# Kernel tuning notes

Hardware: AMD Instinct MI355X
Metric: run time of the kernel (lower is better)

The kernel has to match this reference:

```python
import jax, jax.numpy as jnp
import numpy as np

N, E, T, D = 50000, 800000, 400000, 64


def _linear_params(key, fan_in, fan_out):
    kw, kb = jax.random.split(key)
    s = 1.0 / np.sqrt(fan_in)
    W = jax.random.uniform(kw, (fan_in, fan_out), minval=-s, maxval=s, dtype=jnp.float32)
    b = jax.random.uniform(kb, (fan_out,), minval=-s, maxval=s, dtype=jnp.float32)
    return W, b


def setup_inputs() -> dict:
    key = jax.random.key(0)
    ks = jax.random.split(key, 11)
    Ws1, bs1 = _linear_params(ks[0], 2 * D, D)
    Ws2, bs2 = _linear_params(ks[1], D, 3 * D)
    Wc1, bc1 = _linear_params(ks[2], 2 * D, D)
    Wc2, bc2 = _linear_params(ks[3], D, D)
    WV, bV = _linear_params(ks[4], D, D)
    return {
        "node_scalar": jax.random.normal(ks[5], (N, D), dtype=jnp.float32),
        "node_chiral": jax.random.normal(ks[6], (N, D), dtype=jnp.float32),
        "node_vector": jax.random.normal(ks[7], (N, 3, D), dtype=jnp.float32),
        "pos": jax.random.normal(ks[8], (N, 3), dtype=jnp.float32),
        "edge_index": jax.random.randint(ks[9], (E, 2), 0, N, dtype=jnp.int64),
        "triplet_index": jax.random.randint(ks[10], (T, 4), 0, N, dtype=jnp.int64),
        "Ws1": Ws1, "bs1": bs1, "Ws2": Ws2, "bs2": bs2,
        "Wc1": Wc1, "bc1": bc1, "Wc2": Wc2, "bc2": bc2,
        "WV": WV, "bV": bV,
    }


def reference(node_scalar, node_chiral, node_vector, pos, edge_index, triplet_index,
              Ws1, bs1, Ws2, bs2, Wc1, bc1, Wc2, bc2, WV, bV):
    n = node_scalar.shape[0]
    d = node_scalar.shape[1]
    e0, e1 = edge_index[:, 0], edge_index[:, 1]

    # Scalar / vector section: gather -> Linear-SiLU-Linear gate -> scatter-add
    g = jax.nn.silu(jnp.concatenate([node_scalar[e0], node_scalar[e1]], axis=1) @ Ws1 + bs1) @ Ws2 + bs2
    gate_vector, gate_edge, messages_ss = jnp.split(g, 3, axis=1)  # each [E, d]
    messages_vv = gate_vector[:, None, :] * node_vector[e1]               # [E, 3, d]
    rel = pos[e1] - pos[e0]                                               # [E, 3]
    messages_ev = gate_edge[:, None, :] * rel[:, :, None]                 # [E, 3, d]
    msg_ss = jax.ops.segment_sum(messages_ss, e0, num_segments=n)
    msg_vv = jax.ops.segment_sum(messages_vv, e0, num_segments=n)
    msg_ev = jax.ops.segment_sum(messages_ev, e0, num_segments=n)

    Vv = node_vector @ WV + bV          # [N, 3, d]
    Vv_norm = jnp.linalg.norm(Vv, axis=1)  # [N, d] (norm over spatial axis)
    message_vs = node_scalar * Vv_norm

    # Chiral section: triplet gathers, shared gate MLP, scalar triple product
    base, t1, t2, t3 = (triplet_index[:, i] for i in range(4))
    hc_base = node_chiral[base]

    def cgate(other):
        h = jnp.concatenate([hc_base, node_chiral[other]], axis=1)
        return jax.nn.silu(h @ Wc1 + bc1) @ Wc2 + bc2

    chiral_gate = cgate(t1) + cgate(t2) + cgate(t3)  # [T, d]
    pb = pos[base]
    r1, r2, r3 = pb - pos[t1], pb - pos[t2], pb - pos[t3]
    stp = jnp.einsum('ei,ei->e', r1, jnp.cross(r2, r3))  # scalar triple product [T]
    chiral_messages = chiral_gate / (stp + 0.01)[:, None]
    msg_chiral = jax.ops.segment_sum(chiral_messages, base, num_segments=n)

    return (node_scalar + msg_ss + message_vs,
            node_chiral + msg_chiral,
            node_vector + msg_vv + msg_ev)
```

## Files before the change

### kernel.cpp

```cpp
#include <hip/hip_runtime.h>
#include <math.h>

#define DD 64
typedef unsigned short ushort_t;
typedef __attribute__((ext_vector_type(8))) short bf16x8;
typedef __attribute__((ext_vector_type(4))) float f32x4;

__device__ __forceinline__ float silu_f(float x) {
    return x / (1.0f + __expf(-x));
}

__device__ __forceinline__ unsigned f32_to_bf16_rne(float x) {
    unsigned u = __float_as_uint(x);
    unsigned r = ((u >> 16) & 1u) + 0x7fffu;
    return (u + r) >> 16;
}

__device__ __forceinline__ float bf16_to_f32(ushort_t v) {
    return __uint_as_float(((unsigned)v) << 16);
}

__device__ __forceinline__ float2 bf2_lo_hi(unsigned u) {
    return make_float2(__uint_as_float(u << 16), __uint_as_float(u & 0xffff0000u));
}

__device__ __forceinline__ void gload_lds4(const void* gsrc, void* lds_base) {
    __builtin_amdgcn_global_load_lds(
        (const __attribute__((address_space(1))) void*)gsrc,
        (__attribute__((address_space(3))) void*)lds_base,
        4, 0, 0);
}

#define RFL(x) __builtin_amdgcn_readfirstlane(x)

__global__ __launch_bounds__(256) void hist_kernel(const int* __restrict__ eidx,
                                                   int* __restrict__ counts, int E) {
    int i = blockIdx.x * 256 + threadIdx.x;
    if (i < E) atomicAdd(&counts[((const int2*)eidx)[i].x], 1);
}

__global__ __launch_bounds__(1024) void scan_kernel(const int* __restrict__ counts,
                                                    int* __restrict__ cursor, int N) {
    __shared__ int part[1024];
    int tid = threadIdx.x;
    int CH = (N + 1023) / 1024;
    int lo = tid * CH, hi = lo + CH; if (hi > N) hi = N; if (lo > N) lo = N;
    int s = 0;
    for (int i = lo; i < hi; ++i) s += counts[i];
    part[tid] = s;
    __syncthreads();
    for (int d = 1; d < 1024; d <<= 1) {
        int v = (tid >= d) ? part[tid - d] : 0;
        __syncthreads();
        part[tid] += v;
        __syncthreads();
    }
    int run = (tid == 0) ? 0 : part[tid - 1];
    for (int i = lo; i < hi; ++i) {
        cursor[i] = run;
        run += counts[i];
    }
}

__global__ __launch_bounds__(256) void scatter2_kernel(const int* __restrict__ eidx,
                                                       const float* __restrict__ pos,
                                                       int* __restrict__ cursor,
                                                       int2* __restrict__ eperm,
                                                       float* __restrict__ relg, int E) {
    int i = blockIdx.x * 256 + threadIdx.x;
    if (i < E) {
        int2 p = ((const int2*)eidx)[i];
        int dst = atomicAdd(&cursor[p.x], 1);
        eperm[dst] = p;
        relg[3 * (size_t)dst + 0] = pos[(size_t)p.y * 3 + 0] - pos[(size_t)p.x * 3 + 0];
        relg[3 * (size_t)dst + 1] = pos[(size_t)p.y * 3 + 1] - pos[(size_t)p.x * 3 + 1];
        relg[3 * (size_t)dst + 2] = pos[(size_t)p.y * 3 + 2] - pos[(size_t)p.x * 3 + 2];
    }
}

__global__ __launch_bounds__(256) void node_transform_kernel(
    const float* __restrict__ ns, const float* __restrict__ nc,
    const float* __restrict__ Ws1, const float* __restrict__ Wc1,
    ushort_t* __restrict__ Abf, ushort_t* __restrict__ Bbf,
    float* __restrict__ C, float* __restrict__ Dm,
    float* __restrict__ out1, int N)
{
    __shared__ float w1[128 * 64];
    __shared__ float wc1s[128 * 64];
    __shared__ float xs[4][2][64];
    __shared__ float ys[4][2][64];
    int tid = threadIdx.x;
    for (int i = tid; i < 128 * 64 / 4; i += 256) {
        ((float4*)w1)[i]   = ((const float4*)Ws1)[i];
        ((float4*)wc1s)[i] = ((const float4*)Wc1)[i];
    }
    __syncthreads();
    int wave = tid >> 6, lane = tid & 63;
    for (int nb = blockIdx.x * 8; nb < N; nb += gridDim.x * 8) {
        int n0 = nb + wave * 2;
        #pragma unroll
        for (int s = 0; s < 2; ++s) {
            int n = n0 + s;
            float xv = 0.f, yv = 0.f;
            if (n < N) { xv = ns[(size_t)n * DD + lane]; yv = nc[(size_t)n * DD + lane]; }
            xs[wave][s][lane] = xv;
            ys[wave][s][lane] = yv;
        }
        float aA[2] = {0.f, 0.f}, aB[2] = {0.f, 0.f}, aC[2] = {0.f, 0.f}, aD[2] = {0.f, 0.f};
        for (int k = 0; k < 64; ++k) {
            float wa  = w1[k * 64 + lane];
            float wb  = w1[(64 + k) * 64 + lane];
            float wca = wc1s[k * 64 + lane];
            float wcb = wc1s[(64 + k) * 64 + lane];
            #pragma unroll
            for (int s = 0; s < 2; ++s) {
                float xk = xs[wave][s][k];
                float yk = ys[wave][s][k];
                aA[s] += xk * wa;  aB[s] += xk * wb;
                aC[s] += yk * wca; aD[s] += yk * wcb;
            }
        }
        #pragma unroll
        for (int s = 0; s < 2; ++s) {
            int n = n0 + s;
            if (n < N) {
                Abf[(size_t)n * DD + lane] = (ushort_t)f32_to_bf16_rne(aA[s]);
                Bbf[(size_t)n * DD + lane] = (ushort_t)f32_to_bf16_rne(aB[s]);
                C[(size_t)n * DD + lane]  = aC[s];
                Dm[(size_t)n * DD + lane] = aD[s];
                out1[(size_t)n * DD + lane] = ys[wave][s][lane];
            }
        }
    }
}

__global__ __launch_bounds__(256) void node_vector_kernel(
    const float* __restrict__ ns, const float* __restrict__ nv,
    const float* __restrict__ WV, const float* __restrict__ bV,
    float* __restrict__ out0, float* __restrict__ out2,
    unsigned* __restrict__ nv01p, ushort_t* __restrict__ nv2bf, int N)
{
    __shared__ float wv[64 * 64];
    __shared__ float vs[4][2][3][64];
    int tid = threadIdx.x;
    for (int i = tid; i < 64 * 64 / 4; i += 256)
        ((float4*)wv)[i] = ((const float4*)WV)[i];
    __syncthreads();
    int wave = tid >> 6, lane = tid & 63;
    float bVj = bV[lane];
    for (int nb = blockIdx.x * 8; nb < N; nb += gridDim.x * 8) {
        int n0 = nb + wave * 2;
        #pragma unroll
        for (int s = 0; s < 2; ++s) {
            int n = n0 + s;
            float v0 = 0.f, v1 = 0.f, v2 = 0.f;
            if (n < N) {
                v0 = nv[((size_t)n * 3 + 0) * DD + lane];
                v1 = nv[((size_t)n * 3 + 1) * DD + lane];
                v2 = nv[((size_t)n * 3 + 2) * DD + lane];
            }
            vs[wave][s][0][lane] = v0; vs[wave][s][1][lane] = v1; vs[wave][s][2][lane] = v2;
        }
        float a0[2], a1[2], a2[2];
        #pragma unroll
        for (int s = 0; s < 2; ++s) { a0[s] = bVj; a1[s] = bVj; a2[s] = bVj; }
        for (int k = 0; k < 64; ++k) {
            float w = wv[k * 64 + lane];
            #pragma unroll
            for (int s = 0; s < 2; ++s) {
                a0[s] += vs[wave][s][0][k] * w;
                a1[s] += vs[wave][s][1][k] * w;
                a2[s] += vs[wave][s][2][k] * w;
            }
        }
        #pragma unroll
        for (int s = 0; s < 2; ++s) {
            int n = n0 + s;
            if (n < N) {
                float norm = sqrtf(a0[s] * a0[s] + a1[s] * a1[s] + a2[s] * a2[s]);
                float x = ns[(size_t)n * DD + lane];
                out0[(size_t)n * DD + lane] = x * (1.f + norm);
                float v0 = vs[wave][s][0][lane], v1 = vs[wave][s][1][lane], v2 = vs[wave][s][2][lane];
                out2[((size_t)n * 3 + 0) * DD + lane] = v0;
                out2[((size_t)n * 3 + 1) * DD + lane] = v1;
                out2[((size_t)n * 3 + 2) * DD + lane] = v2;
                nv01p[(size_t)n * DD + lane] = f32_to_bf16_rne(v0) | (f32_to_bf16_rne(v1) << 16);
                nv2bf[(size_t)n * DD + lane] = (ushort_t)f32_to_bf16_rne(v2);
            }
        }
    }
}

#define GEPW 16
__global__ __launch_bounds__(256) void edge_kernel(
    const ushort_t* __restrict__ Abf, const ushort_t* __restrict__ Bbf,
    const unsigned* __restrict__ nv01p, const ushort_t* __restrict__ nv2bf,
    const float* __restrict__ relg, const int2* __restrict__ eperm,
    const float* __restrict__ bs1, const float* __restrict__ Ws2, const float* __restrict__ bs2,
    float* __restrict__ out0, float* __restrict__ out2, int E)
{
    __shared__ unsigned w2frag[12 * 2 * 64 * 4];
    __shared__ ushort_t stAB[4][GEPW][128];
    __shared__ ushort_t stNV2[4][GEPW / 2][132];
    __shared__ float    relL[4][64];
    int tid = threadIdx.x;
    for (int i = tid; i < 12 * 2 * 64; i += 256) {
        int t  = i >> 7;
        int kk = (i >> 6) & 1;
        int l  = i & 63;
        int k0 = kk * 32 + (l >> 4) * 8;
        int col = t * 16 + (l & 15);
        #pragma unroll
        for (int jp = 0; jp < 4; ++jp) {
            float a = Ws2[(size_t)(k0 + 2 * jp) * 192 + col];
            float b = Ws2[(size_t)(k0 + 2 * jp + 1) * 192 + col];
            w2frag[i * 4 + jp] = f32_to_bf16_rne(a) | (f32_to_bf16_rne(b) << 16);
        }
    }
    __syncthreads();
    int wave = RFL(tid >> 6);
    int lane = tid & 63;
    float b1 = bs1[lane];
    float b2v_t[4], b2e_t[4], b2s_t[4];
    #pragma unroll
    for (int t = 0; t < 4; ++t) {
        b2v_t[t] = bs2[t * 16 + (lane & 15)];
        b2e_t[t] = bs2[64 + t * 16 + (lane & 15)];
        b2s_t[t] = bs2[128 + t * 16 + (lane & 15)];
    }

    int bid = blockIdx.x;
    int cpx = (int)(gridDim.x >> 3);
    int swz = (bid & 7) * cpx + (bid >> 3);

    long nG = ((long)E + GEPW - 1) / GEPW;
    for (long g = (long)swz * 4 + wave; g < nG; g += (long)gridDim.x * 4) {
        long e0b = g * GEPW;
        int i0a[GEPW], i1a[GEPW];
        #pragma unroll
        for (int e = 0; e < GEPW; ++e) {
            long eid = e0b + e; if (eid >= E) eid = E - 1;
            int2 p = eperm[eid];
            i0a[e] = RFL(p.x); i1a[e] = RFL(p.y);
        }
        int vi_all = 0, vi1_all = 0;
        #pragma unroll
        for (int e = 0; e < GEPW; ++e) {
            vi_all  = (lane == e) ? i0a[e] : vi_all;
            vi1_all = (lane == e) ? i1a[e] : vi1_all;
        }
        #pragma unroll
        for (int e = 0; e < GEPW; ++e) {
            const char* srcAB = (lane < 32)
                ? ((const char*)Abf + (size_t)i0a[e] * 128 + lane * 4)
                : ((const char*)Bbf + (size_t)i1a[e] * 128 + (lane - 32) * 4);
            gload_lds4(srcAB, &stAB[wave][e][0]);
        }
        __builtin_amdgcn_sched_barrier(0);
        #pragma unroll
        for (int p2 = 0; p2 < GEPW / 2; ++p2) {
            const char* src2 = (lane < 32)
                ? ((const char*)nv2bf + (size_t)i1a[2 * p2] * 128 + lane * 4)
                : ((const char*)nv2bf + (size_t)i1a[2 * p2 + 1] * 128 + (lane - 32) * 4);
            gload_lds4(src2, &stNV2[wave][p2][0]);
        }
        gload_lds4((const char*)relg + e0b * 12 + lane * 4, &relL[wave][0]);
        int eL0 = (lane >> 4) * 4;
        unsigned nv01r[4][4];
        #pragma unroll
        for (int rg = 0; rg < 4; ++rg) {
            int i1s = __builtin_amdgcn_ds_bpermute((eL0 + rg) * 4, vi1_all);
            const char* basep = (const char*)nv01p + (size_t)(unsigned)i1s * 256 + (lane & 15) * 4;
            nv01r[rg][0] = *(const unsigned*)(basep);
            nv01r[rg][1] = *(const unsigned*)(basep + 64);
            nv01r[rg][2] = *(const unsigned*)(basep + 128);
            nv01r[rg][3] = *(const unsigned*)(basep + 192);
        }
        __builtin_amdgcn_sched_barrier(0);
        asm volatile("s_waitcnt vmcnt(25)" ::: "memory");
        __builtin_amdgcn_sched_barrier(0);
        #pragma unroll
        for (int e = 0; e < GEPW; ++e) {
            float a = bf16_to_f32(stAB[wave][e][lane]);
            float b = bf16_to_f32(stAB[wave][e][64 + lane]);
            float h = silu_f(a + b + b1);
            *(float*)((char*)&stAB[wave][e][0] + ((lane * 4) ^ ((e & 7) << 5))) = h;
        }
        __builtin_amdgcn_sched_barrier(0);
        f32x4 acc[12];
        f32x4 zz = {0.f, 0.f, 0.f, 0.f};
        #pragma unroll
        for (int t = 0; t < 12; ++t) acc[t] = zz;
        int row = lane & 15;
        #pragma unroll
        for (int kk = 0; kk < 2; ++kk) {
            int coff = (kk * 128 + ((lane >> 4) * 32)) ^ ((row & 7) << 5);
            const char* hp = (const char*)&stAB[wave][row][0] + coff;
            float4 lo = *(const float4*)hp;
            float4 hi = *(const float4*)(hp + 16);
            unsigned a0, a1, a2, a3;
            asm("v_cvt_pk_bf16_f32 %0, %1, %2" : "=v"(a0) : "v"(lo.x), "v"(lo.y));
            asm("v_cvt_pk_bf16_f32 %0, %1, %2" : "=v"(a1) : "v"(lo.z), "v"(lo.w));
            asm("v_cvt_pk_bf16_f32 %0, %1, %2" : "=v"(a2) : "v"(hi.x), "v"(hi.y));
            asm("v_cvt_pk_bf16_f32 %0, %1, %2" : "=v"(a3) : "v"(hi.z), "v"(hi.w));
            union { unsigned u[4]; bf16x8 v; } af;
            af.u[0] = a0; af.u[1] = a1; af.u[2] = a2; af.u[3] = a3;
            #pragma unroll
            for (int t = 0; t < 12; ++t) {
                bf16x8 bf = *(const bf16x8*)&w2frag[((t * 2 + kk) * 64 + lane) * 4];
                acc[t] = __builtin_amdgcn_mfma_f32_16x16x32_bf16(af.v, bf, acc[t], 0, 0, 0);
            }
        }
        asm volatile("s_waitcnt vmcnt(0)" ::: "memory");
        __builtin_amdgcn_sched_barrier(0);
        float aS[4]  = {0.f, 0.f, 0.f, 0.f};
        float aV0[4] = {0.f, 0.f, 0.f, 0.f};
        float aV1[4] = {0.f, 0.f, 0.f, 0.f};
        float aV2[4] = {0.f, 0.f, 0.f, 0.f};
        int icur = __builtin_amdgcn_ds_bpermute(eL0 * 4, vi_all);
        #pragma unroll
        for (int rg = 0; rg < 4; ++rg) {
            int e = eL0 + rg;
            int i0 = __builtin_amdgcn_ds_bpermute(e * 4, vi_all);
            bool ok = (e0b + e) < E;
            if (i0 != icur) {
                #pragma unroll
                for (int t = 0; t < 4; ++t) {
                    int dim = t * 16 + (lane & 15);
                    unsafeAtomicAdd(&out0[(size_t)(unsigned)icur * 64u + dim], aS[t]);
                    unsafeAtomicAdd(&out2[((size_t)(unsigned)icur * 3u + 0) * 64u + dim], aV0[t]);
                    unsafeAtomicAdd(&out2[((size_t)(unsigned)icur * 3u + 1) * 64u + dim], aV1[t]);
                    unsafeAtomicAdd(&out2[((size_t)(unsigned)icur * 3u + 2) * 64u + dim], aV2[t]);
                    aS[t] = 0.f; aV0[t] = 0.f; aV1[t] = 0.f; aV2[t] = 0.f;
                }
                icur = i0;
            }
            if (ok) {
                float r0v = relL[wave][e * 3 + 0];
                float r1v = relL[wave][e * 3 + 1];
                float r2v = relL[wave][e * 3 + 2];
                #pragma unroll
                for (int t = 0; t < 4; ++t) {
                    int dim = t * 16 + (lane & 15);
                    float gv = acc[t][rg]     + b2v_t[t];
                    float ge = acc[4 + t][rg] + b2e_t[t];
                    float ss = acc[8 + t][rg] + b2s_t[t];
                    float2 vv = bf2_lo_hi(nv01r[rg][t]);
                    float v2 = bf16_to_f32(stNV2[wave][e >> 1][(e & 1) * 64 + dim]);
                    aS[t]  += ss;
                    aV0[t] += gv * vv.x + ge * r0v;
                    aV1[t] += gv * vv.y + ge * r1v;
                    aV2[t] += gv * v2   + ge * r2v;
                }
            }
        }
        #pragma unroll
        for (int t = 0; t < 4; ++t) {
            int dim = t * 16 + (lane & 15);
            unsafeAtomicAdd(&out0[(size_t)(unsigned)icur * 64u + dim], aS[t]);
            unsafeAtomicAdd(&out2[((size_t)(unsigned)icur * 3u + 0) * 64u + dim], aV0[t]);
            unsafeAtomicAdd(&out2[((size_t)(unsigned)icur * 3u + 1) * 64u + dim], aV1[t]);
            unsafeAtomicAdd(&out2[((size_t)(unsigned)icur * 3u + 2) * 64u + dim], aV2[t]);
        }
    }
}

#define TPW 8
__global__ __launch_bounds__(256) void triplet_kernel(
    const float* __restrict__ C, const float* __restrict__ Dm,
    const float* __restrict__ pos, const int* __restrict__ tidx,
    const float* __restrict__ bc1, const float* __restrict__ Wc2, const float* __restrict__ bc2,
    float* __restrict__ out1, int T)
{
    __shared__ float wT[64 * 64];
    __shared__ float stC[4][TPW][64];
    __shared__ float stD[4][TPW][3][64];
    int tid = threadIdx.x;
    for (int i = tid; i < 64 * 64 / 4; i += 256)
        ((float4*)wT)[i] = ((const float4*)Wc2)[i];
    __syncthreads();
    int wave = RFL(tid >> 6);
    int lane = tid & 63;
    float b1 = bc1[lane];
    float b2 = bc2[lane] * 3.0f;
    for (long bb = (long)blockIdx.x * (4 * TPW); bb < T; bb += (long)gridDim.x * (4 * TPW)) {
        long t0 = bb + wave * TPW;
        int ib[TPW], it1[TPW], it2[TPW], it3[TPW];
        #pragma unroll
        for (int e = 0; e < TPW; ++e) {
            long t = t0 + e;
            int b = 0, t1 = 0, t2 = 0, t3 = 0;
            if (t < T) { int4 q = ((const int4*)tidx)[t]; b = q.x; t1 = q.y; t2 = q.z; t3 = q.w; }
            ib[e]  = RFL(b);
            it1[e] = RFL(t1);
            it2[e] = RFL(t2);
            it3[e] = RFL(t3);
        }
        #pragma unroll
        for (int e = 0; e < TPW; ++e) {
            gload_lds4(C  + (size_t)ib[e]  * DD + lane, &stC[wave][e][0]);
            gload_lds4(Dm + (size_t)it1[e] * DD + lane, &stD[wave][e][0][0]);
            gload_lds4(Dm + (size_t)it2[e] * DD + lane, &stD[wave][e][1][0]);
            gload_lds4(Dm + (size_t)it3[e] * DD + lane, &stD[wave][e][2][0]);
        }
        asm volatile("s_waitcnt vmcnt(0)" ::: "memory");
        float inv[TPW];
        #pragma unroll
        for (int e = 0; e < TPW; ++e) {
            float hb = stC[wave][e][lane] + b1;
            float h = silu_f(hb + stD[wave][e][0][lane])
                    + silu_f(hb + stD[wave][e][1][lane])
                    + silu_f(hb + stD[wave][e][2][lane]);
            stC[wave][e][lane] = h;
            int b = ib[e], t1 = it1[e], t2 = it2[e], t3 = it3[e];
            double pbx = pos[(size_t)b * 3], pby = pos[(size_t)b * 3 + 1], pbz = pos[(size_t)b * 3 + 2];
            double r1x = pbx - pos[(size_t)t1 * 3], r1y = pby - pos[(size_t)t1 * 3 + 1], r1z = pbz - pos[(size_t)t1 * 3 + 2];
            double r2x = pbx - pos[(size_t)t2 * 3], r2y = pby - pos[(size_t)t2 * 3 + 1], r2z = pbz - pos[(size_t)t2 * 3 + 2];
            double r3x = pbx - pos[(size_t)t3 * 3], r3y = pby - pos[(size_t)t3 * 3 + 1], r3z = pbz - pos[(size_t)t3 * 3 + 2];
            double cx = r2y * r3z - r2z * r3y;
            double cy = r2z * r3x - r2x * r3z;
            double cz = r2x * r3y - r2y * r3x;
            double stp = r1x * cx + r1y * cy + r1z * cz;
            inv[e] = (float)(1.0 / (stp + 0.01));
        }
        float acc[TPW];
        #pragma unroll
        for (int e = 0; e < TPW; ++e) acc[e] = 0.f;
        for (int k4 = 0; k4 < 64; k4 += 4) {
            float4 hk[TPW];
            #pragma unroll
            for (int e = 0; e < TPW; ++e) hk[e] = *(const float4*)&stC[wave][e][k4];
            #pragma unroll
            for (int kk = 0; kk < 4; ++kk) {
                float wk = wT[(k4 + kk) * 64 + lane];
                #pragma unroll
                for (int e = 0; e < TPW; ++e) acc[e] += (&hk[e].x)[kk] * wk;
            }
        }
        #pragma unroll
        for (int e = 0; e < TPW; ++e) {
            long t = t0 + e;
            if (t >= T) break;
            unsafeAtomicAdd(&out1[(size_t)ib[e] * DD + lane], (acc[e] + b2) * inv[e]);
        }
    }
}

extern "C" void kernel_launch(void* const* d_in, const int* in_sizes, int n_in,
                              void* d_out, int out_size, void* d_ws, size_t ws_size,
                              hipStream_t stream)
{
    const float* ns  = (const float*)d_in[0];
    const float* nc  = (const float*)d_in[1];
    const float* nv  = (const float*)d_in[2];
    const float* pos = (const float*)d_in[3];
    const int* eidx  = (const int*)d_in[4];
    const int* tidx  = (const int*)d_in[5];
    const float* Ws1 = (const float*)d_in[6];
    const float* bs1 = (const float*)d_in[7];
    const float* Ws2 = (const float*)d_in[8];
    const float* bs2 = (const float*)d_in[9];
    const float* Wc1 = (const float*)d_in[10];
    const float* bc1 = (const float*)d_in[11];
    const float* Wc2 = (const float*)d_in[12];
    const float* bc2 = (const float*)d_in[13];
    const float* WV  = (const float*)d_in[14];
    const float* bV  = (const float*)d_in[15];

    int N = in_sizes[0] / 64;
    int E = in_sizes[4] / 2;
    int T = in_sizes[5] / 4;

    float* out0 = (float*)d_out;
    float* out1 = out0 + (size_t)N * 64;
    float* out2 = out1 + (size_t)N * 64;

    float* C    = (float*)d_ws;
    float* Dm   = C + (size_t)N * 64;
    float* relg = Dm + (size_t)N * 64;
    int2* eperm = (int2*)(relg + (size_t)E * 3 + 64);
    int* counts = (int*)(eperm + (size_t)E);
    int* cursor = counts + N;
    unsigned* nv01p = (unsigned*)(cursor + N);
    ushort_t* Abf   = (ushort_t*)(nv01p + (size_t)N * 64);
    ushort_t* Bbf   = Abf + (size_t)N * 64;
    ushort_t* nv2bf = Bbf + (size_t)N * 64;

    hipMemsetAsync(counts, 0, (size_t)N * sizeof(int), stream);
    hist_kernel<<<(E + 255) / 256, 256, 0, stream>>>(eidx, counts, E);
    scan_kernel<<<1, 1024, 0, stream>>>(counts, cursor, N);
    scatter2_kernel<<<(E + 255) / 256, 256, 0, stream>>>(eidx, pos, cursor, eperm, relg, E);
    node_transform_kernel<<<2048, 256, 0, stream>>>(ns, nc, Ws1, Wc1, Abf, Bbf, C, Dm, out1, N);
    node_vector_kernel<<<2048, 256, 0, stream>>>(ns, nv, WV, bV, out0, out2, nv01p, nv2bf, N);
    edge_kernel<<<4096, 256, 0, stream>>>(Abf, Bbf, nv01p, nv2bf, relg, eperm, bs1, Ws2, bs2, out0, out2, E);
    triplet_kernel<<<2048, 256, 0, stream>>>(C, Dm, pos, tidx, bc1, Wc2, bc2, out1, T);
}
```

Before: 953.6 us.

## Merge independent kernels into block-partitioned fused launches

Scatter, node-transform and node-vector kernels become one launch whose blocks pick a role by block index. The edge and triplet kernels are likewise merged into one launch, so independent work runs concurrently and fewer launches are needed. The cost is a large shared-memory footprint sized for the biggest role, which may lower occupancy for the lighter roles. The node loops also gain an extra __syncthreads per iteration.

Result: slower. 994.6 us (+4.3%).

```diff
diff --git a/kernel.cpp b/kernel.cpp
--- a/kernel.cpp
+++ b/kernel.cpp
@@ -5,6 +5,11 @@
 typedef unsigned short ushort_t;
 typedef __attribute__((ext_vector_type(8))) short bf16x8;
 typedef __attribute__((ext_vector_type(4))) float f32x4;
+
+#define GEPW 16
+#define TPW 8
+#define EGRID 4096
+#define TGRID 2048
 
 __device__ __forceinline__ float silu_f(float x) {
     return x / (1.0f + __expf(-x));
@@ -62,386 +67,395 @@
     }
 }
 
-__global__ __launch_bounds__(256) void scatter2_kernel(const int* __restrict__ eidx,
-                                                       const float* __restrict__ pos,
-                                                       int* __restrict__ cursor,
-                                                       int2* __restrict__ eperm,
-                                                       float* __restrict__ relg, int E) {
-    int i = blockIdx.x * 256 + threadIdx.x;
-    if (i < E) {
-        int2 p = ((const int2*)eidx)[i];
-        int dst = atomicAdd(&cursor[p.x], 1);
-        eperm[dst] = p;
-        relg[3 * (size_t)dst + 0] = pos[(size_t)p.y * 3 + 0] - pos[(size_t)p.x * 3 + 0];
-        relg[3 * (size_t)dst + 1] = pos[(size_t)p.y * 3 + 1] - pos[(size_t)p.x * 3 + 1];
-        relg[3 * (size_t)dst + 2] = pos[(size_t)p.y * 3 + 2] - pos[(size_t)p.x * 3 + 2];
-    }
-}
-
-__global__ __launch_bounds__(256) void node_transform_kernel(
+__global__ __launch_bounds__(256) void fused_prep_kernel(
+    const int* __restrict__ eidx, const float* __restrict__ pos,
+    int* __restrict__ cursor, int2* __restrict__ eperm, float* __restrict__ relg,
     const float* __restrict__ ns, const float* __restrict__ nc,
     const float* __restrict__ Ws1, const float* __restrict__ Wc1,
     ushort_t* __restrict__ Abf, ushort_t* __restrict__ Bbf,
-    float* __restrict__ C, float* __restrict__ Dm,
-    float* __restrict__ out1, int N)
+    float* __restrict__ C, float* __restrict__ Dm, float* __restrict__ out1,
+    const float* __restrict__ nv, const float* __restrict__ WV, const float* __restrict__ bV,
+    float* __restrict__ out0, float* __restrict__ out2,
+    unsigned* __restrict__ nv01p, ushort_t* __restrict__ nv2bf,
+    int N, int E, int sblocks)
 {
-    __shared__ float w1[128 * 64];
-    __shared__ float wc1s[128 * 64];
-    __shared__ float xs[4][2][64];
-    __shared__ float ys[4][2][64];
+    __shared__ __align__(16) char smem[69632];
     int tid = threadIdx.x;
-    for (int i = tid; i < 128 * 64 / 4; i += 256) {
-        ((float4*)w1)[i]   = ((const float4*)Ws1)[i];
-        ((float4*)wc1s)[i] = ((const float4*)Wc1)[i];
-    }
-    __syncthreads();
-    int wave = tid >> 6, lane = tid & 63;
-    for (int nb = blockIdx.x * 8; nb < N; nb += gridDim.x * 8) {
-        int n0 = nb + wave * 2;
-        #pragma unroll
-        for (int s = 0; s < 2; ++s) {
-            int n = n0 + s;
-            float xv = 0.f, yv = 0.f;
-            if (n < N) { xv = ns[(size_t)n * DD + lane]; yv = nc[(size_t)n * DD + lane]; }
-            xs[wave][s][lane] = xv;
-            ys[wave][s][lane] = yv;
-        }
-        float aA[2] = {0.f, 0.f}, aB[2] = {0.f, 0.f}, aC[2] = {0.f, 0.f}, aD[2] = {0.f, 0.f};
-        for (int k = 0; k < 64; ++k) {
-            float wa  = w1[k * 64 + lane];
-            float wb  = w1[(64 + k) * 64 + lane];
-            float wca = wc1s[k * 64 + lane];
-            float wcb = wc1s[(64 + k) * 64 + lane];
+    int bx = blockIdx.x;
+
+    if (bx < sblocks) {
+        int i = bx * 256 + tid;
+        if (i < E) {
+            int2 p = ((const int2*)eidx)[i];
+            int dst = atomicAdd(&cursor[p.x], 1);
+            eperm[dst] = p;
+            relg[3 * (size_t)dst + 0] = pos[(size_t)p.y * 3 + 0] - pos[(size_t)p.x * 3 + 0];
+            relg[3 * (size_t)dst + 1] = pos[(size_t)p.y * 3 + 1] - pos[(size_t)p.x * 3 + 1];
+            relg[3 * (size_t)dst + 2] = pos[(size_t)p.y * 3 + 2] - pos[(size_t)p.x * 3 + 2];
+        }
+        return;
+    }
+    if (bx < sblocks + 2048) {
+        int blk = bx - sblocks;
+        float* w1   = (float*)smem;
+        float* wc1s = (float*)(smem + 32768);
+        float* xs   = (float*)(smem + 65536);
+        float* ys   = (float*)(smem + 67584);
+        for (int i = tid; i < 128 * 64 / 4; i += 256) {
+            ((float4*)w1)[i]   = ((const float4*)Ws1)[i];
+            ((float4*)wc1s)[i] = ((const float4*)Wc1)[i];
+        }
+        __syncthreads();
+        int wave = tid >> 6, lane = tid & 63;
+        for (int nb = blk * 8; nb < N; nb += 2048 * 8) {
+            int n0 = nb + wave * 2;
             #pragma unroll
             for (int s = 0; s < 2; ++s) {
-                float xk = xs[wave][s][k];
-                float yk = ys[wave][s][k];
-                aA[s] += xk * wa;  aB[s] += xk * wb;
-                aC[s] += yk * wca; aD[s] += yk * wcb;
-            }
-        }
-        #pragma unroll
-        for (int s = 0; s < 2; ++s) {
-            int n = n0 + s;
-            if (n < N) {
-                Abf[(size_t)n * DD + lane] = (ushort_t)f32_to_bf16_rne(aA[s]);
-                Bbf[(size_t)n * DD + lane] = (ushort_t)f32_to_bf16_rne(aB[s]);
-                C[(size_t)n * DD + lane]  = aC[s];
-                Dm[(size_t)n * DD + lane] = aD[s];
-                out1[(size_t)n * DD + lane] = ys[wave][s][lane];
-            }
-        }
-    }
-}
-
-__global__ __launch_bounds__(256) void node_vector_kernel(
-    const float* __restrict__ ns, const float* __restrict__ nv,
-    const float* __restrict__ WV, const float* __restrict__ bV,
-    float* __restrict__ out0, float* __restrict__ out2,
-    unsigned* __restrict__ nv01p, ushort_t* __restrict__ nv2bf, int N)
-{
-    __shared__ float wv[64 * 64];
-    __shared__ float vs[4][2][3][64];
-    int tid = threadIdx.x;
-    for (int i = tid; i < 64 * 64 / 4; i += 256)
-        ((float4*)wv)[i] = ((const float4*)WV)[i];
-    __syncthreads();
-    int wave = tid >> 6, lane = tid & 63;
-    float bVj = bV[lane];
-    for (int nb = blockIdx.x * 8; nb < N; nb += gridDim.x * 8) {
-        int n0 = nb + wave * 2;
-        #pragma unroll
-        for (int s = 0; s < 2; ++s) {
-            int n = n0 + s;
-            float v0 = 0.f, v1 = 0.f, v2 = 0.f;
-            if (n < N) {
-                v0 = nv[((size_t)n * 3 + 0) * DD + lane];
-                v1 = nv[((size_t)n * 3 + 1) * DD + lane];
-                v2 = nv[((size_t)n * 3 + 2) * DD + lane];
-            }
-            vs[wave][s][0][lane] = v0; vs[wave][s][1][lane] = v1; vs[wave][s][2][lane] = v2;
-        }
-        float a0[2], a1[2], a2[2];
-        #pragma unroll
-        for (int s = 0; s < 2; ++s) { a0[s] = bVj; a1[s] = bVj; a2[s] = bVj; }
-        for (int k = 0; k < 64; ++k) {
-            float w = wv[k * 64 + lane];
+                int n = n0 + s;
+                float xv = 0.f, yv = 0.f;
+                if (n < N) { xv = ns[(size_t)n * DD + lane]; yv = nc[(size_t)n * DD + lane]; }
+                xs[(wave * 2 + s) * 64 + lane] = xv;
+                ys[(wave * 2 + s) * 64 + lane] = yv;
+            }
+            float aA[2] = {0.f, 0.f}, aB[2] = {0.f, 0.f}, aC[2] = {0.f, 0.f}, aD[2] = {0.f, 0.f};
+            for (int k = 0; k < 64; ++k) {
+                float wa  = w1[k * 64 + lane];
+                float wb  = w1[(64 + k) * 64 + lane];
+                float wca = wc1s[k * 64 + lane];
+                float wcb = wc1s[(64 + k) * 64 + lane];
+                #pragma unroll
+                for (int s = 0; s < 2; ++s) {
+                    float xk = xs[(wave * 2 + s) * 64 + k];
+                    float yk = ys[(wave * 2 + s) * 64 + k];
+                    aA[s] += xk * wa;  aB[s] += xk * wb;
+                    aC[s] += yk * wca; aD[s] += yk * wcb;
+                }
+            }
             #pragma unroll
             for (int s = 0; s < 2; ++s) {
-                a0[s] += vs[wave][s][0][k] * w;
-                a1[s] += vs[wave][s][1][k] * w;
-                a2[s] += vs[wave][s][2][k] * w;
-            }
-        }
-        #pragma unroll
-        for (int s = 0; s < 2; ++s) {
-            int n = n0 + s;
-            if (n < N) {
-                float norm = sqrtf(a0[s] * a0[s] + a1[s] * a1[s] + a2[s] * a2[s]);
-                float x = ns[(size_t)n * DD + lane];
-                out0[(size_t)n * DD + lane] = x * (1.f + norm);
-                float v0 = vs[wave][s][0][lane], v1 = vs[wave][s][1][lane], v2 = vs[wave][s][2][lane];
-                out2[((size_t)n * 3 + 0) * DD + lane] = v0;
-                out2[((size_t)n * 3 + 1) * DD + lane] = v1;
-                out2[((size_t)n * 3 + 2) * DD + lane] = v2;
-                nv01p[(size_t)n * DD + lane] = f32_to_bf16_rne(v0) | (f32_to_bf16_rne(v1) << 16);
-                nv2bf[(size_t)n * DD + lane] = (ushort_t)f32_to_bf16_rne(v2);
-            }
-        }
-    }
-}
-
-#define GEPW 16
-__global__ __launch_bounds__(256) void edge_kernel(
+                int n = n0 + s;
+                if (n < N) {
+                    Abf[(size_t)n * DD + lane] = (ushort_t)f32_to_bf16_rne(aA[s]);
+                    Bbf[(size_t)n * DD + lane] = (ushort_t)f32_to_bf16_rne(aB[s]);
+                    C[(size_t)n * DD + lane]  = aC[s];
+                    Dm[(size_t)n * DD + lane] = aD[s];
+                    out1[(size_t)n * DD + lane] = ys[(wave * 2 + s) * 64 + lane];
+                }
+            }
+            __syncthreads();
+        }
+        return;
+    }
+    {
+        int blk = bx - sblocks - 2048;
+        float* wv = (float*)smem;
+        float* vs = (float*)(smem + 16384);
+        for (int i = tid; i < 64 * 64 / 4; i += 256)
+            ((float4*)wv)[i] = ((const float4*)WV)[i];
+        __syncthreads();
+        int wave = tid >> 6, lane = tid & 63;
+        float bVj = bV[lane];
+        for (int nb = blk * 8; nb < N; nb += 2048 * 8) {
+            int n0 = nb + wave * 2;
+            #pragma unroll
+            for (int s = 0; s < 2; ++s) {
+                int n = n0 + s;
+                float v0 = 0.f, v1 = 0.f, v2 = 0.f;
+                if (n < N) {
+                    v0 = nv[((size_t)n * 3 + 0) * DD + lane];
+                    v1 = nv[((size_t)n * 3 + 1) * DD + lane];
+                    v2 = nv[((size_t)n * 3 + 2) * DD + lane];
+                }
+                vs[((wave * 2 + s) * 3 + 0) * 64 + lane] = v0;
+                vs[((wave * 2 + s) * 3 + 1) * 64 + lane] = v1;
+                vs[((wave * 2 + s) * 3 + 2) * 64 + lane] = v2;
+            }
+            float a0[2], a1[2], a2[2];
+            #pragma unroll
+            for (int s = 0; s < 2; ++s) { a0[s] = bVj; a1[s] = bVj; a2[s] = bVj; }
+            for (int k = 0; k < 64; ++k) {
+                float w = wv[k * 64 + lane];
+                #pragma unroll
+                for (int s = 0; s < 2; ++s) {
+                    a0[s] += vs[((wave * 2 + s) * 3 + 0) * 64 + k] * w;
+                    a1[s] += vs[((wave * 2 + s) * 3 + 1) * 64 + k] * w;
+                    a2[s] += vs[((wave * 2 + s) * 3 + 2) * 64 + k] * w;
+                }
+            }
+            #pragma unroll
+            for (int s = 0; s < 2; ++s) {
+                int n = n0 + s;
+                if (n < N) {
+                    float norm = sqrtf(a0[s] * a0[s] + a1[s] * a1[s] + a2[s] * a2[s]);
+                    float x = ns[(size_t)n * DD + lane];
+                    out0[(size_t)n * DD + lane] = x * (1.f + norm);
+                    float v0 = vs[((wave * 2 + s) * 3 + 0) * 64 + lane];
+                    float v1 = vs[((wave * 2 + s) * 3 + 1) * 64 + lane];
+                    float v2 = vs[((wave * 2 + s) * 3 + 2) * 64 + lane];
+                    out2[((size_t)n * 3 + 0) * DD + lane] = v0;
+                    out2[((size_t)n * 3 + 1) * DD + lane] = v1;
+                    out2[((size_t)n * 3 + 2) * DD + lane] = v2;
+                    nv01p[(size_t)n * DD + lane] = f32_to_bf16_rne(v0) | (f32_to_bf16_rne(v1) << 16);
+                    nv2bf[(size_t)n * DD + lane] = (ushort_t)f32_to_bf16_rne(v2);
+                }
+            }
+            __syncthreads();
+        }
+    }
+}
+
+__global__ __launch_bounds__(256) void fused_et_kernel(
     const ushort_t* __restrict__ Abf, const ushort_t* __restrict__ Bbf,
     const unsigned* __restrict__ nv01p, const ushort_t* __restrict__ nv2bf,
     const float* __restrict__ relg, const int2* __restrict__ eperm,
     const float* __restrict__ bs1, const float* __restrict__ Ws2, const float* __restrict__ bs2,
-    float* __restrict__ out0, float* __restrict__ out2, int E)
-{
-    __shared__ unsigned w2frag[12 * 2 * 64 * 4];
-    __shared__ ushort_t stAB[4][GEPW][128];
-    __shared__ ushort_t stNV2[4][GEPW / 2][132];
-    __shared__ float    relL[4][64];
-    int tid = threadIdx.x;
-    for (int i = tid; i < 12 * 2 * 64; i += 256) {
-        int t  = i >> 7;
-        int kk = (i >> 6) & 1;
-        int l  = i & 63;
-        int k0 = kk * 32 + (l >> 4) * 8;
-        int col = t * 16 + (l & 15);
-        #pragma unroll
-        for (int jp = 0; jp < 4; ++jp) {
-            float a = Ws2[(size_t)(k0 + 2 * jp) * 192 + col];
-            float b = Ws2[(size_t)(k0 + 2 * jp + 1) * 192 + col];
-            w2frag[i * 4 + jp] = f32_to_bf16_rne(a) | (f32_to_bf16_rne(b) << 16);
-        }
-    }
-    __syncthreads();
-    int wave = RFL(tid >> 6);
-    int lane = tid & 63;
-    float b1 = bs1[lane];
-    float b2v_t[4], b2e_t[4], b2s_t[4];
-    #pragma unroll
-    for (int t = 0; t < 4; ++t) {
-        b2v_t[t] = bs2[t * 16 + (lane & 15)];
-        b2e_t[t] = bs2[64 + t * 16 + (lane & 15)];
-        b2s_t[t] = bs2[128 + t * 16 + (lane & 15)];
-    }
-
-    int bid = blockIdx.x;
-    int cpx = (int)(gridDim.x >> 3);
-    int swz = (bid & 7) * cpx + (bid >> 3);
-
-    long nG = ((long)E + GEPW - 1) / GEPW;
-    for (long g = (long)swz * 4 + wave; g < nG; g += (long)gridDim.x * 4) {
-        long e0b = g * GEPW;
-        int i0a[GEPW], i1a[GEPW];
-        #pragma unroll
-        for (int e = 0; e < GEPW; ++e) {
-            long eid = e0b + e; if (eid >= E) eid = E - 1;
-            int2 p = eperm[eid];
-            i0a[e] = RFL(p.x); i1a[e] = RFL(p.y);
-        }
-        int vi_all = 0, vi1_all = 0;
-        #pragma unroll
-        for (int e = 0; e < GEPW; ++e) {
-            vi_all  = (lane == e) ? i0a[e] : vi_all;
-            vi1_all = (lane == e) ? i1a[e] : vi1_all;
-        }
-        #pragma unroll
-        for (int e = 0; e < GEPW; ++e) {
-            const char* srcAB = (lane < 32)
-                ? ((const char*)Abf + (size_t)i0a[e] * 128 + lane * 4)
-                : ((const char*)Bbf + (size_t)i1a[e] * 128 + (lane - 32) * 4);
-            gload_lds4(srcAB, &stAB[wave][e][0]);
-        }
-        __builtin_amdgcn_sched_barrier(0);
-        #pragma unroll
-        for (int p2 = 0; p2 < GEPW / 2; ++p2) {
-            const char* src2 = (lane < 32)
-                ? ((const char*)nv2bf + (size_t)i1a[2 * p2] * 128 + lane * 4)
-                : ((const char*)nv2bf + (size_t)i1a[2 * p2 + 1] * 128 + (lane - 32) * 4);
-            gload_lds4(src2, &stNV2[wave][p2][0]);
-        }
-        gload_lds4((const char*)relg + e0b * 12 + lane * 4, &relL[wave][0]);
-        int eL0 = (lane >> 4) * 4;
-        unsigned nv01r[4][4];
-        #pragma unroll
-        for (int rg = 0; rg < 4; ++rg) {
-            int i1s = __builtin_amdgcn_ds_bpermute((eL0 + rg) * 4, vi1_all);
-            const char* basep = (const char*)nv01p + (size_t)(unsigned)i1s * 256 + (lane & 15) * 4;
-            nv01r[rg][0] = *(const unsigned*)(basep);
-            nv01r[rg][1] = *(const unsigned*)(basep + 64);
-            nv01r[rg][2] = *(const unsigned*)(basep + 128);
-            nv01r[rg][3] = *(const unsigned*)(basep + 192);
-        }
-        __builtin_amdgcn_sched_barrier(0);
-        asm volatile("s_waitcnt vmcnt(25)" ::: "memory");
-        __builtin_amdgcn_sched_barrier(0);
-        #pragma unroll
-        for (int e = 0; e < GEPW; ++e) {
-            float a = bf16_to_f32(stAB[wave][e][lane]);
-            float b = bf16_to_f32(stAB[wave][e][64 + lane]);
-            float h = silu_f(a + b + b1);
-            *(float*)((char*)&stAB[wave][e][0] + ((lane * 4) ^ ((e & 7) << 5))) = h;
-        }
-        __builtin_amdgcn_sched_barrier(0);
-        f32x4 acc[12];
-        f32x4 zz = {0.f, 0.f, 0.f, 0.f};
-        #pragma unroll
-        for (int t = 0; t < 12; ++t) acc[t] = zz;
-        int row = lane & 15;
-        #pragma unroll
-        for (int kk = 0; kk < 2; ++kk) {
-            int coff = (kk * 128 + ((lane >> 4) * 32)) ^ ((row & 7) << 5);
-            const char* hp = (const char*)&stAB[wave][row][0] + coff;
-            float4 lo = *(const float4*)hp;
-            float4 hi = *(const float4*)(hp + 16);
-            unsigned a0, a1, a2, a3;
-            asm("v_cvt_pk_bf16_f32 %0, %1, %2" : "=v"(a0) : "v"(lo.x), "v"(lo.y));
-            asm("v_cvt_pk_bf16_f32 %0, %1, %2" : "=v"(a1) : "v"(lo.z), "v"(lo.w));
-            asm("v_cvt_pk_bf16_f32 %0, %1, %2" : "=v"(a2) : "v"(hi.x), "v"(hi.y));
-            asm("v_cvt_pk_bf16_f32 %0, %1, %2" : "=v"(a3) : "v"(hi.z), "v"(hi.w));
-            union { unsigned u[4]; bf16x8 v; } af;
-            af.u[0] = a0; af.u[1] = a1; af.u[2] = a2; af.u[3] = a3;
-            #pragma unroll
-            for (int t = 0; t < 12; ++t) {
-                bf16x8 bf = *(const bf16x8*)&w2frag[((t * 2 + kk) * 64 + lane) * 4];
-                acc[t] = __builtin_amdgcn_mfma_f32_16x16x32_bf16(af.v, bf, acc[t], 0, 0, 0);
-            }
-        }
-        asm volatile("s_waitcnt vmcnt(0)" ::: "memory");
-        __builtin_amdgcn_sched_barrier(0);
-        float aS[4]  = {0.f, 0.f, 0.f, 0.f};
-        float aV0[4] = {0.f, 0.f, 0.f, 0.f};
-        float aV1[4] = {0.f, 0.f, 0.f, 0.f};
-        float aV2[4] = {0.f, 0.f, 0.f, 0.f};
-        int icur = __builtin_amdgcn_ds_bpermute(eL0 * 4, vi_all);
-        #pragma unroll
-        for (int rg = 0; rg < 4; ++rg) {
-            int e = eL0 + rg;
-            int i0 = __builtin_amdgcn_ds_bpermute(e * 4, vi_all);
-            bool ok = (e0b + e) < E;
-            if (i0 != icur) {
-                #pragma unroll
-                for (int t = 0; t < 4; ++t) {
-                    int dim = t * 16 + (lane & 15);
-                    unsafeAtomicAdd(&out0[(size_t)(unsigned)icur * 64u + dim], aS[t]);
-                    unsafeAtomicAdd(&out2[((size_t)(unsigned)icur * 3u + 0) * 64u + dim], aV0[t]);
-                    unsafeAtomicAdd(&out2[((size_t)(unsigned)icur * 3u + 1) * 64u + dim], aV1[t]);
-                    unsafeAtomicAdd(&out2[((size_t)(unsigned)icur * 3u + 2) * 64u + dim], aV2[t]);
-                    aS[t] = 0.f; aV0[t] = 0.f; aV1[t] = 0.f; aV2[t] = 0.f;
-                }
-                icur = i0;
-            }
-            if (ok) {
-                float r0v = relL[wave][e * 3 + 0];
-                float r1v = relL[wave][e * 3 + 1];
-                float r2v = relL[wave][e * 3 + 2];
-                #pragma unroll
-                for (int t = 0; t < 4; ++t) {
-                    int dim = t * 16 + (lane & 15);
-                    float gv = acc[t][rg]     + b2v_t[t];
-                    float ge = acc[4 + t][rg] + b2e_t[t];
-                    float ss = acc[8 + t][rg] + b2s_t[t];
-                    float2 vv = bf2_lo_hi(nv01r[rg][t]);
-                    float v2 = bf16_to_f32(stNV2[wave][e >> 1][(e & 1) * 64 + dim]);
-                    aS[t]  += ss;
-                    aV0[t] += gv * vv.x + ge * r0v;
-                    aV1[t] += gv * vv.y + ge * r1v;
-                    aV2[t] += gv * v2   + ge * r2v;
-                }
-            }
-        }
-        #pragma unroll
-        for (int t = 0; t < 4; ++t) {
-            int dim = t * 16 + (lane & 15);
-            unsafeAtomicAdd(&out0[(size_t)(unsigned)icur * 64u + dim], aS[t]);
-            unsafeAtomicAdd(&out2[((size_t)(unsigned)icur * 3u + 0) * 64u + dim], aV0[t]);
-            unsafeAtomicAdd(&out2[((size_t)(unsigned)icur * 3u + 1) * 64u + dim], aV1[t]);
-            unsafeAtomicAdd(&out2[((size_t)(unsigned)icur * 3u + 2) * 64u + dim], aV2[t]);
-        }
-    }
-}
-
-#define TPW 8
-__global__ __launch_bounds__(256) void triplet_kernel(
     const float* __restrict__ C, const float* __restrict__ Dm,
     const float* __restrict__ pos, const int* __restrict__ tidx,
     const float* __restrict__ bc1, const float* __restrict__ Wc2, const float* __restrict__ bc2,
-    float* __restrict__ out1, int T)
+    float* __restrict__ out0, float* __restrict__ out1, float* __restrict__ out2,
+    int E, int T)
 {
-    __shared__ float wT[64 * 64];
-    __shared__ float stC[4][TPW][64];
-    __shared__ float stD[4][TPW][3][64];
+    __shared__ __align__(16) char smem[50432];
     int tid = threadIdx.x;
-    for (int i = tid; i < 64 * 64 / 4; i += 256)
-        ((float4*)wT)[i] = ((const float4*)Wc2)[i];
-    __syncthreads();
-    int wave = RFL(tid >> 6);
-    int lane = tid & 63;
-    float b1 = bc1[lane];
-    float b2 = bc2[lane] * 3.0f;
-    for (long bb = (long)blockIdx.x * (4 * TPW); bb < T; bb += (long)gridDim.x * (4 * TPW)) {
-        long t0 = bb + wave * TPW;
-        int ib[TPW], it1[TPW], it2[TPW], it3[TPW];
+
+    if (blockIdx.x < EGRID) {
+        unsigned* w2frag = (unsigned*)smem;
+        ushort_t* stAB   = (ushort_t*)(smem + 24576);
+        ushort_t* stNV2  = (ushort_t*)(smem + 40960);
+        float*    relL   = (float*)(smem + 49408);
+        for (int i = tid; i < 12 * 2 * 64; i += 256) {
+            int t  = i >> 7;
+            int kk = (i >> 6) & 1;
+            int l  = i & 63;
+            int k0 = kk * 32 + (l >> 4) * 8;
+            int col = t * 16 + (l & 15);
+            #pragma unroll
+            for (int jp = 0; jp < 4; ++jp) {
+                float a = Ws2[(size_t)(k0 + 2 * jp) * 192 + col];
+                float b = Ws2[(size_t)(k0 + 2 * jp + 1) * 192 + col];
+                w2frag[i * 4 + jp] = f32_to_bf16_rne(a) | (f32_to_bf16_rne(b) << 16);
+            }
+        }
+        __syncthreads();
+        int wave = RFL(tid >> 6);
+        int lane = tid & 63;
+        float b1 = bs1[lane];
+        float b2v_t[4], b2e_t[4], b2s_t[4];
         #pragma unroll
-        for (int e = 0; e < TPW; ++e) {
-            long t = t0 + e;
-            int b = 0, t1 = 0, t2 = 0, t3 = 0;
-            if (t < T) { int4 q = ((const int4*)tidx)[t]; b = q.x; t1 = q.y; t2 = q.z; t3 = q.w; }
-            ib[e]  = RFL(b);
-            it1[e] = RFL(t1);
-            it2[e] = RFL(t2);
-            it3[e] = RFL(t3);
-        }
-        #pragma unroll
-        for (int e = 0; e < TPW; ++e) {
-            gload_lds4(C  + (size_t)ib[e]  * DD + lane, &stC[wave][e][0]);
-            gload_lds4(Dm + (size_t)it1[e] * DD + lane, &stD[wave][e][0][0]);
-            gload_lds4(Dm + (size_t)it2[e] * DD + lane, &stD[wave][e][1][0]);
-            gload_lds4(Dm + (size_t)it3[e] * DD + lane, &stD[wave][e][2][0]);
-        }
-        asm volatile("s_waitcnt vmcnt(0)" ::: "memory");
-        float inv[TPW];
-        #pragma unroll
-        for (int e = 0; e < TPW; ++e) {
-            float hb = stC[wave][e][lane] + b1;
-            float h = silu_f(hb + stD[wave][e][0][lane])
-                    + silu_f(hb + stD[wave][e][1][lane])
-                    + silu_f(hb + stD[wave][e][2][lane]);
-            stC[wave][e][lane] = h;
-            int b = ib[e], t1 = it1[e], t2 = it2[e], t3 = it3[e];
-            double pbx = pos[(size_t)b * 3], pby = pos[(size_t)b * 3 + 1], pbz = pos[(size_t)b * 3 + 2];
-            double r1x = pbx - pos[(size_t)t1 * 3], r1y = pby - pos[(size_t)t1 * 3 + 1], r1z = pbz - pos[(size_t)t1 * 3 + 2];
-            double r2x = pbx - pos[(size_t)t2 * 3], r2y = pby - pos[(size_t)t2 * 3 + 1], r2z = pbz - pos[(size_t)t2 * 3 + 2];
-            double r3x = pbx - pos[(size_t)t3 * 3], r3y = pby - pos[(size_t)t3 * 3 + 1], r3z = pbz - pos[(size_t)t3 * 3 + 2];
-            double cx = r2y * r3z - r2z * r3y;
-            double cy = r2z * r3x - r2x * r3z;
-            double cz = r2x * r3y - r2y * r3x;
-            double stp = r1x * cx + r1y * cy + r1z * cz;
-            inv[e] = (float)(1.0 / (stp + 0.01));
-        }
-        float acc[TPW];
-        #pragma unroll
-        for (int e = 0; e < TPW; ++e) acc[e] = 0.f;
-        for (int k4 = 0; k4 < 64; k4 += 4) {
-            float4 hk[TPW];
-            #pragma unroll
-            for (int e = 0; e < TPW; ++e) hk[e] = *(const float4*)&stC[wave][e][k4];
-            #pragma unroll
-            for (int kk = 0; kk < 4; ++kk) {
-                float wk = wT[(k4 + kk) * 64 + lane];
+        for (int t = 0; t < 4; ++t) {
+            b2v_t[t] = bs2[t * 16 + (lane & 15)];
+            b2e_t[t] = bs2[64 + t * 16 + (lane & 15)];
+            b2s_t[t] = bs2[128 + t * 16 + (lane & 15)];
+        }
+        int bid = blockIdx.x;
+        int cpx = EGRID >> 3;
+        int swz = (bid & 7) * cpx + (bid >> 3);
+
+        long nG = ((long)E + GEPW - 1) / GEPW;
+        for (long g = (long)swz * 4 + wave; g < nG; g += (long)EGRID * 4) {
+            long e0b = g * GEPW;
+            int i0a[GEPW], i1a[GEPW];
+            #pragma unroll
+            for (int e = 0; e < GEPW; ++e) {
+                long eid = e0b + e; if (eid >= E) eid = E - 1;
+                int2 p = eperm[eid];
+                i0a[e] = RFL(p.x); i1a[e] = RFL(p.y);
+            }
+            int vi_all = 0, vi1_all = 0;
+            #pragma unroll
+            for (int e = 0; e < GEPW; ++e) {
+                vi_all  = (lane == e) ? i0a[e] : vi_all;
+                vi1_all = (lane == e) ? i1a[e] : vi1_all;
+            }
+            #pragma unroll
+            for (int e = 0; e < GEPW; ++e) {
+                const char* srcAB = (lane < 32)
+                    ? ((const char*)Abf + (size_t)i0a[e] * 128 + lane * 4)
+                    : ((const char*)Bbf + (size_t)i1a[e] * 128 + (lane - 32) * 4);
+                gload_lds4(srcAB, stAB + (wave * GEPW + e) * 128);
+            }
+            __builtin_amdgcn_sched_barrier(0);
+            #pragma unroll
+            for (int p2 = 0; p2 < GEPW / 2; ++p2) {
+                const char* src2 = (lane < 32)
+                    ? ((const char*)nv2bf + (size_t)i1a[2 * p2] * 128 + lane * 4)
+                    : ((const char*)nv2bf + (size_t)i1a[2 * p2 + 1] * 128 + (lane - 32) * 4);
+                gload_lds4(src2, stNV2 + (wave * (GEPW / 2) + p2) * 132);
+            }
+            gload_lds4((const char*)relg + e0b * 12 + lane * 4, relL + wave * 64);
+            int eL0 = (lane >> 4) * 4;
+            unsigned nv01r[4][4];
+            #pragma unroll
+            for (int rg = 0; rg < 4; ++rg) {
+                int i1s = __builtin_amdgcn_ds_bpermute((eL0 + rg) * 4, vi1_all);
+                const char* basep = (const char*)nv01p + (size_t)(unsigned)i1s * 256 + (lane & 15) * 4;
+                nv01r[rg][0] = *(const unsigned*)(basep);
+                nv01r[rg][1] = *(const unsigned*)(basep + 64);
+                nv01r[rg][2] = *(const unsigned*)(basep + 128);
+                nv01r[rg][3] = *(const unsigned*)(basep + 192);
+            }
+            __builtin_amdgcn_sched_barrier(0);
+            asm volatile("s_waitcnt vmcnt(25)" ::: "memory");
+            __builtin_amdgcn_sched_barrier(0);
+            #pragma unroll
+            for (int e = 0; e < GEPW; ++e) {
+                float a = bf16_to_f32(stAB[(wave * GEPW + e) * 128 + lane]);
+                float b = bf16_to_f32(stAB[(wave * GEPW + e) * 128 + 64 + lane]);
+                float h = silu_f(a + b + b1);
+                *(float*)((char*)(stAB + (wave * GEPW + e) * 128) + ((lane * 4) ^ ((e & 7) << 5))) = h;
+            }
+            __builtin_amdgcn_sched_barrier(0);
+            f32x4 acc[12];
+            f32x4 zz = {0.f, 0.f, 0.f, 0.f};
+            #pragma unroll
+            for (int t = 0; t < 12; ++t) acc[t] = zz;
+            int row = lane & 15;
+            #pragma unroll
+            for (int kk = 0; kk < 2; ++kk) {
+                int coff = (kk * 128 + ((lane >> 4) * 32)) ^ ((row & 7) << 5);
+                const char* hp = (const char*)(stAB + (wave * GEPW + row) * 128) + coff;
+                float4 lo = *(const float4*)hp;
+                float4 hi = *(const float4*)(hp + 16);
+                unsigned a0, a1, a2, a3;
+                asm("v_cvt_pk_bf16_f32 %0, %1, %2" : "=v"(a0) : "v"(lo.x), "v"(lo.y));
+                asm("v_cvt_pk_bf16_f32 %0, %1, %2" : "=v"(a1) : "v"(lo.z), "v"(lo.w));
+                asm("v_cvt_pk_bf16_f32 %0, %1, %2" : "=v"(a2) : "v"(hi.x), "v"(hi.y));
+                asm("v_cvt_pk_bf16_f32 %0, %1, %2" : "=v"(a3) : "v"(hi.z), "v"(hi.w));
+                union { unsigned u[4]; bf16x8 v; } af;
+                af.u[0] = a0; af.u[1] = a1; af.u[2] = a2; af.u[3] = a3;
                 #pragma unroll
-                for (int e = 0; e < TPW; ++e) acc[e] += (&hk[e].x)[kk] * wk;
-            }
-        }
-        #pragma unroll
-        for (int e = 0; e < TPW; ++e) {
-            long t = t0 + e;
-            if (t >= T) break;
-            unsafeAtomicAdd(&out1[(size_t)ib[e] * DD + lane], (acc[e] + b2) * inv[e]);
+                for (int t = 0; t < 12; ++t) {
+                    bf16x8 bf = *(const bf16x8*)&w2frag[((t * 2 + kk) * 64 + lane) * 4];
+                    acc[t] = __builtin_amdgcn_mfma_f32_16x16x32_bf16(af.v, bf, acc[t], 0, 0, 0);
+                }
+            }
+            asm volatile("s_waitcnt vmcnt(0)" ::: "memory");
+            __builtin_amdgcn_sched_barrier(0);
+            float aS[4]  = {0.f, 0.f, 0.f, 0.f};
+            float aV0[4] = {0.f, 0.f, 0.f, 0.f};
+            float aV1[4] = {0.f, 0.f, 0.f, 0.f};
+            float aV2[4] = {0.f, 0.f, 0.f, 0.f};
+            int icur = __builtin_amdgcn_ds_bpermute(eL0 * 4, vi_all);
+            #pragma unroll
+            for (int rg = 0; rg < 4; ++rg) {
+                int e = eL0 + rg;
+                int i0 = __builtin_amdgcn_ds_bpermute(e * 4, vi_all);
+                bool ok = (e0b + e) < E;
+                if (i0 != icur) {
+                    #pragma unroll
+                    for (int t = 0; t < 4; ++t) {
+                        int dim = t * 16 + (lane & 15);
+                        unsafeAtomicAdd(&out0[(size_t)(unsigned)icur * 64u + dim], aS[t]);
+                        unsafeAtomicAdd(&out2[((size_t)(unsigned)icur * 3u + 0) * 64u + dim], aV0[t]);
+                        unsafeAtomicAdd(&out2[((size_t)(unsigned)icur * 3u + 1) * 64u + dim], aV1[t]);
+                        unsafeAtomicAdd(&out2[((size_t)(unsigned)icur * 3u + 2) * 64u + dim], aV2[t]);
+                        aS[t] = 0.f; aV0[t] = 0.f; aV1[t] = 0.f; aV2[t] = 0.f;
+                    }
+                    icur = i0;
+                }
+                if (ok) {
+                    float r0v = relL[wave * 64 + e * 3 + 0];
+                    float r1v = relL[wave * 64 + e * 3 + 1];
+                    float r2v = relL[wave * 64 + e * 3 + 2];
+                    #pragma unroll
+                    for (int t = 0; t < 4; ++t) {
+                        int dim = t * 16 + (lane & 15);
+                        float gv = acc[t][rg]     + b2v_t[t];
+                        float ge = acc[4 + t][rg] + b2e_t[t];
+                        float ss = acc[8 + t][rg] + b2s_t[t];
+                        float2 vv = bf2_lo_hi(nv01r[rg][t]);
+                        float v2 = bf16_to_f32(stNV2[(wave * (GEPW / 2) + (e >> 1)) * 132 + (e & 1) * 64 + dim]);
+                        aS[t]  += ss;
+                        aV0[t] += gv * vv.x + ge * r0v;
+                        aV1[t] += gv * vv.y + ge * r1v;
+                        aV2[t] += gv * v2   + ge * r2v;
+                    }
+                }
+            }
+            #pragma unroll
+            for (int t = 0; t < 4; ++t) {
+                int dim = t * 16 + (lane & 15);
+                unsafeAtomicAdd(&out0[(size_t)(unsigned)icur * 64u + dim], aS[t]);
+                unsafeAtomicAdd(&out2[((size_t)(unsigned)icur * 3u + 0) * 64u + dim], aV0[t]);
+                unsafeAtomicAdd(&out2[((size_t)(unsigned)icur * 3u + 1) * 64u + dim], aV1[t]);
+                unsafeAtomicAdd(&out2[((size_t)(unsigned)icur * 3u + 2) * 64u + dim], aV2[t]);
+            }
+        }
+        return;
+    }
+
+    {
+        float* wT  = (float*)smem;
+        float* stC = (float*)(smem + 16384);
+        float* stD = (float*)(smem + 24576);
+        for (int i = tid; i < 64 * 64 / 4; i += 256)
+            ((float4*)wT)[i] = ((const float4*)Wc2)[i];
+        __syncthreads();
+        int wave = RFL(tid >> 6);
+        int lane = tid & 63;
+        float b1 = bc1[lane];
+        float b2 = bc2[lane] * 3.0f;
+        long tb = blockIdx.x - EGRID;
+        for (long bb = tb * (4 * TPW); bb < T; bb += (long)TGRID * (4 * TPW)) {
+            long t0 = bb + wave * TPW;
+            int ib[TPW], it1[TPW], it2[TPW], it3[TPW];
+            #pragma unroll
+            for (int e = 0; e < TPW; ++e) {
+                long t = t0 + e;
+                int b = 0, t1 = 0, t2 = 0, t3 = 0;
+                if (t < T) { int4 q = ((const int4*)tidx)[t]; b = q.x; t1 = q.y; t2 = q.z; t3 = q.w; }
+                ib[e]  = RFL(b);
+                it1[e] = RFL(t1);
+                it2[e] = RFL(t2);
+                it3[e] = RFL(t3);
+            }
+            #pragma unroll
+            for (int e = 0; e < TPW; ++e) {
+                gload_lds4(C  + (size_t)ib[e]  * DD + lane, stC + (wave * TPW + e) * 64);
+                gload_lds4(Dm + (size_t)it1[e] * DD + lane, stD + ((wave * TPW + e) * 3 + 0) * 64);
+                gload_lds4(Dm + (size_t)it2[e] * DD + lane, stD + ((wave * TPW + e) * 3 + 1) * 64);
+                gload_lds4(Dm + (size_t)it3[e] * DD + lane, stD + ((wave * TPW + e) * 3 + 2) * 64);
+            }
+            asm volatile("s_waitcnt vmcnt(0)" ::: "memory");
+            float inv[TPW];
+            #pragma unroll
+            for (int e = 0; e < TPW; ++e) {
+                float hb = stC[(wave * TPW + e) * 64 + lane] + b1;
+                float h = silu_f(hb + stD[((wave * TPW + e) * 3 + 0) * 64 + lane])
+                        + silu_f(hb + stD[((wave * TPW + e) * 3 + 1) * 64 + lane])
+                        + silu_f(hb + stD[((wave * TPW + e) * 3 + 2) * 64 + lane]);
+                stC[(wave * TPW + e) * 64 + lane] = h;
+                int b = ib[e], t1 = it1[e], t2 = it2[e], t3 = it3[e];
+                double pbx = pos[(size_t)b * 3], pby = pos[(size_t)b * 3 + 1], pbz = pos[(size_t)b * 3 + 2];
+                double r1x = pbx - pos[(size_t)t1 * 3], r1y = pby - pos[(size_t)t1 * 3 + 1], r1z = pbz - pos[(size_t)t1 * 3 + 2];
+                double r2x = pbx - pos[(size_t)t2 * 3], r2y = pby - pos[(size_t)t2 * 3 + 1], r2z = pbz - pos[(size_t)t2 * 3 + 2];
+                double r3x = pbx - pos[(size_t)t3 * 3], r3y = pby - pos[(size_t)t3 * 3 + 1], r3z = pbz - pos[(size_t)t3 * 3 + 2];
+                double cx = r2y * r3z - r2z * r3y;
+                double cy = r2z * r3x - r2x * r3z;
+                double cz = r2x * r3y - r2y * r3x;
+                double stp = r1x * cx + r1y * cy + r1z * cz;
+                inv[e] = (float)(1.0 / (stp + 0.01));
+            }
+            float acc[TPW];
+            #pragma unroll
+            for (int e = 0; e < TPW; ++e) acc[e] = 0.f;
+            for (int k4 = 0; k4 < 64; k4 += 4) {
+                float4 hk[TPW];
+                #pragma unroll
+                for (int e = 0; e < TPW; ++e) hk[e] = *(const float4*)&stC[(wave * TPW + e) * 64 + k4];
+                #pragma unroll
+                for (int kk = 0; kk < 4; ++kk) {
+                    float wk = wT[(k4 + kk) * 64 + lane];
+                    #pragma unroll
+                    for (int e = 0; e < TPW; ++e) acc[e] += (&hk[e].x)[kk] * wk;
+                }
+            }
+            #pragma unroll
+            for (int e = 0; e < TPW; ++e) {
+                long t = t0 + e;
+                if (t >= T) break;
+                unsafeAtomicAdd(&out1[(size_t)ib[e] * DD + lane], (acc[e] + b2) * inv[e]);
+            }
         }
     }
 }
@@ -486,12 +500,19 @@
     ushort_t* Bbf   = Abf + (size_t)N * 64;
     ushort_t* nv2bf = Bbf + (size_t)N * 64;
 
+    int sblocks = (E + 255) / 256;
+
     hipMemsetAsync(counts, 0, (size_t)N * sizeof(int), stream);
-    hist_kernel<<<(E + 255) / 256, 256, 0, stream>>>(eidx, counts, E);
+    hist_kernel<<<sblocks, 256, 0, stream>>>(eidx, counts, E);
     scan_kernel<<<1, 1024, 0, stream>>>(counts, cursor, N);
-    scatter2_kernel<<<(E + 255) / 256, 256, 0, stream>>>(eidx, pos, cursor, eperm, relg, E);
-    node_transform_kernel<<<2048, 256, 0, stream>>>(ns, nc, Ws1, Wc1, Abf, Bbf, C, Dm, out1, N);
-    node_vector_kernel<<<2048, 256, 0, stream>>>(ns, nv, WV, bV, out0, out2, nv01p, nv2bf, N);
-    edge_kernel<<<4096, 256, 0, stream>>>(Abf, Bbf, nv01p, nv2bf, relg, eperm, bs1, Ws2, bs2, out0, out2, E);
-    triplet_kernel<<<2048, 256, 0, stream>>>(C, Dm, pos, tidx, bc1, Wc2, bc2, out1, T);
-}
+    fused_prep_kernel<<<sblocks + 4096, 256, 0, stream>>>(
+        eidx, pos, cursor, eperm, relg,
+        ns, nc, Ws1, Wc1, Abf, Bbf, C, Dm, out1,
+        nv, WV, bV, out0, out2, nv01p, nv2bf,
+        N, E, sblocks);
+    fused_et_kernel<<<EGRID + TGRID, 256, 0, stream>>>(
+        Abf, Bbf, nv01p, nv2bf, relg, eperm,
+        bs1, Ws2, bs2,
+        C, Dm, pos, tidx, bc1, Wc2, bc2,
+        out0, out1, out2, E, T);
+}
```
